# Kernel optimization log

Hardware: AMD Instinct MI355X
Metric: run time of the kernel (lower is better)

## Reference

```python
import jax, jax.numpy as jnp
import numpy as np

N_NODES = 50000
N_EDGES = 800000
D = 128


def setup_inputs() -> dict:
    key = jax.random.key(0)
    ks = jax.random.split(key, 8)
    scale = 1.0 / np.sqrt(D)
    return {
        "x": jax.random.normal(ks[0], (N_NODES, D), jnp.float32),
        "src": jax.random.randint(ks[1], (N_EDGES,), 0, N_NODES, jnp.int64 if jax.config.jax_enable_x64 else jnp.int32),
        "dst": jax.random.randint(ks[2], (N_EDGES,), 0, N_NODES, jnp.int64 if jax.config.jax_enable_x64 else jnp.int32),
        "W_self0": jax.random.normal(ks[3], (D, D), jnp.float32) * scale,
        "W_neigh0": jax.random.normal(ks[4], (D, D), jnp.float32) * scale,
        "b0": jnp.zeros((D,), jnp.float32),
        "W_self1": jax.random.normal(ks[5], (D, D), jnp.float32) * scale,
        "W_neigh1": jax.random.normal(ks[6], (D, D), jnp.float32) * scale,
        "b1": jnp.zeros((D,), jnp.float32),
    }


def _sage_conv(h, src, dst, W_self, W_neigh, b, n_nodes):
    # mean aggregation over incoming edges (DGL copy_u + mean; isolated nodes -> 0)
    msg = h[src]                                             # [E, d]
    agg = jax.ops.segment_sum(msg, dst, num_segments=n_nodes)  # [N, d]
    deg = jax.ops.segment_sum(jnp.ones((src.shape[0],), h.dtype), dst, num_segments=n_nodes)
    h_neigh = agg / jnp.maximum(deg, 1.0)[:, None]
    return h @ W_self + h_neigh @ W_neigh + b


def reference(x, src, dst, W_self0, W_neigh0, b0, W_self1, W_neigh1, b1):
    n = x.shape[0]
    h = jax.nn.relu(_sage_conv(x, src, dst, W_self0, W_neigh0, b0, n))
    h = jax.nn.relu(_sage_conv(h, src, dst, W_self1, W_neigh1, b1, n))
    # torch F.normalize(p=2, dim=1): x / max(||x||_2, eps)
    norm = jnp.sqrt(jnp.sum(h * h, axis=1, keepdims=True))
    return h / jnp.maximum(norm, 1e-12)
```

## Files before the change

### kernel.cpp

```cpp
#include <hip/hip_runtime.h>

#define NN 50000
#define D 128
#define BM 32
#define SL 6250
#define CE 1664

typedef unsigned int uint;
typedef unsigned short ushort;
typedef __attribute__((ext_vector_type(8))) short bf16x8;
typedef __attribute__((ext_vector_type(4))) float f32x4;

static __device__ __forceinline__ ushort f2bf(float f) {
    uint u = __float_as_uint(f);
    u = (u + 0x7FFFu + ((u >> 16) & 1u)) >> 16;
    return (ushort)u;
}

#define ADD8(a, u)                                                  \
    {                                                               \
        a[0] += __uint_as_float((u).x << 16);                       \
        a[1] += __uint_as_float((u).x & 0xFFFF0000u);               \
        a[2] += __uint_as_float((u).y << 16);                       \
        a[3] += __uint_as_float((u).y & 0xFFFF0000u);               \
        a[4] += __uint_as_float((u).z << 16);                       \
        a[5] += __uint_as_float((u).z & 0xFFFF0000u);               \
        a[6] += __uint_as_float((u).w << 16);                       \
        a[7] += __uint_as_float((u).w & 0xFFFF0000u);               \
    }

static __device__ __forceinline__ int ladr(int r, int ch) {
    return r * D + (((ch) ^ (r & 7)) << 3);
}

__global__ __launch_bounds__(256) void k_hist_s(const int* __restrict__ dst,
                                                int* __restrict__ hist, int E) {
    const int s = blockIdx.x & 7;
    const int lo = s * SL, hi = lo + SL;
    const int bs = blockIdx.x >> 3;
    for (int e = bs * 256 + (int)threadIdx.x; e < E; e += 128 * 256) {
        const int d = dst[e];
        if (d >= lo && d < hi) atomicAdd(&hist[d], 1);
    }
}

__global__ __launch_bounds__(256) void k_bsum(const int* __restrict__ hist,
                                              int* __restrict__ bsum, int n) {
    const int t = threadIdx.x;
    const int i0 = blockIdx.x * 512 + t * 2;
    int s = 0;
    if (i0 < n) s += hist[i0];
    if (i0 + 1 < n) s += hist[i0 + 1];
    #pragma unroll
    for (int o = 1; o < 64; o <<= 1) s += __shfl_xor(s, o);
    __shared__ int wsum[4];
    if ((t & 63) == 0) wsum[t >> 6] = s;
    __syncthreads();
    if (t == 0) bsum[blockIdx.x] = wsum[0] + wsum[1] + wsum[2] + wsum[3];
}

__global__ __launch_bounds__(256) void k_scanapply_f(
    const int* __restrict__ hist, const int* __restrict__ bsum,
    int* __restrict__ row_off, int* __restrict__ cursor, int n, int E, int nb,
    const float* __restrict__ x, ushort* __restrict__ xb,
    const float* __restrict__ W0, const float* __restrict__ W1,
    const float* __restrict__ W2, const float* __restrict__ W3,
    ushort* __restrict__ P)
{
    const int bid = blockIdx.x;
    const int t = threadIdx.x;
    if (bid < nb) {
        const int sb = bid;
        const int lane = t & 63, w = t >> 6;
        __shared__ int red[4], wsum[4], woff[4], baseS;

        int v = (t < nb && t < sb) ? bsum[t] : 0;
        #pragma unroll
        for (int o = 1; o < 64; o <<= 1) v += __shfl_xor(v, o);
        if (lane == 0) red[w] = v;
        __syncthreads();
        if (t == 0) baseS = red[0] + red[1] + red[2] + red[3];
        __syncthreads();
        const int base = baseS;

        const int i0 = sb * 512 + t * 2;
        const int v0 = (i0 < n) ? hist[i0] : 0;
        const int v1 = (i0 + 1 < n) ? hist[i0 + 1] : 0;
        const int s = v0 + v1;
        int inc = s;
        #pragma unroll
        for (int o = 1; o < 64; o <<= 1) { int u = __shfl_up(inc, o); if (lane >= o) inc += u; }
        if (lane == 63) wsum[w] = inc;
        __syncthreads();
        if (t == 0) { int r = 0; for (int k = 0; k < 4; ++k) { woff[k] = r; r += wsum[k]; } }
        __syncthreads();
        const int ex = base + woff[w] + (inc - s);
        if (i0 < n)     { row_off[i0] = ex;          cursor[i0] = ex; }
        if (i0 + 1 < n) { row_off[i0 + 1] = ex + v0; cursor[i0 + 1] = ex + v0; }
        if (sb == 0 && t == 0) row_off[n] = E;
    } else if (bid < nb + 3125) {
        const int tt = (bid - nb) * 256 + t;
        const float4* p = reinterpret_cast<const float4*>(x) + (size_t)tt * 2;
        const float4 v0 = p[0], v1 = p[1];
        uint4 u;
        u.x = (uint)f2bf(v0.x) | ((uint)f2bf(v0.y) << 16);
        u.y = (uint)f2bf(v0.z) | ((uint)f2bf(v0.w) << 16);
        u.z = (uint)f2bf(v1.x) | ((uint)f2bf(v1.y) << 16);
        u.w = (uint)f2bf(v1.z) | ((uint)f2bf(v1.w) << 16);
        reinterpret_cast<uint4*>(xb)[tt] = u;
    } else {
        const int o = (bid - nb - 3125) * 256 + t;
        const int mat = o >> 14;
        const int idx = o & 16383;
        const int kt = idx >> 12;
        const int nn = (idx >> 5) & 127;
        const int ks = idx & 31;
        const float* W = (mat == 0) ? W0 : (mat == 1) ? W1 : (mat == 2) ? W2 : W3;
        P[o] = f2bf(W[(kt * 32 + ks) * D + nn]);
    }
}

__global__ __launch_bounds__(256) void k_fill_s(const int* __restrict__ src,
        const int* __restrict__ dst, int* __restrict__ cursor,
        int* __restrict__ csr, int E) {
    const int s = blockIdx.x & 7;
    const int lo = s * SL, hi = lo + SL;
    const int bs = blockIdx.x >> 3;
    const int stride = (gridDim.x >> 3) * 256;
    for (int e = bs * 256 + (int)threadIdx.x; e < E; e += stride) {
        const int d = dst[e];
        const int sv = src[e];
        if (d >= lo && d < hi) {
            const int p = atomicAdd(&cursor[d], 1);
            csr[p] = sv;
        }
    }
}

template<bool NORM>
__global__ __launch_bounds__(512, 8) void k_sage(
    const ushort* __restrict__ hb,
    const int* __restrict__ csr, const int* __restrict__ row_off,
    const ushort* __restrict__ Wps, const ushort* __restrict__ Wpn,
    const float* __restrict__ bias, ushort* __restrict__ outb,
    float* __restrict__ out, int n, int E)
{
    __shared__ __align__(16) ushort hsb[BM * D];
    __shared__ __align__(16) ushort hnb[BM * D];
    __shared__ float outt[BM * 132];
    __shared__ int csre[CE];
    const int row0 = blockIdx.x * BM;
    const int tid = threadIdx.x;
    const int l = tid & 63;
    const int w = tid >> 6;

    const int rhi = min(row0 + BM, n);
    const int beg0 = row_off[row0];
    const int EB = row_off[rhi] - beg0;
    const bool useLds = (EB <= CE);
    if (useLds) {
        for (int j = tid; j < EB; j += 512) csre[j] = csr[beg0 + j];
    }

    {
        const int r = tid >> 4;
        const int ch = tid & 15;
        const int g = row0 + r;
        uint4 u = make_uint4(0u, 0u, 0u, 0u);
        if (g < n) u = *reinterpret_cast<const uint4*>(hb + (size_t)g * D + ch * 8);
        *reinterpret_cast<uint4*>(&hsb[ladr(r, ch)]) = u;
    }
    __syncthreads();

    {
        const int r = tid >> 4;
        const int ql = tid & 15;
        const int g = row0 + r;
        int i = 0, e = 0;
        if (g < n) { i = row_off[g]; e = row_off[g + 1]; }
        const float invd = (e > i) ? 1.0f / (float)(e - i) : 0.0f;
        float a[8];
        #pragma unroll
        for (int j = 0; j < 8; ++j) a[j] = 0.f;
        const size_t off = (size_t)(ql * 8);
        if (useLds) {
            int li = i - beg0;
            const int le = e - beg0;
            for (; li + 3 < le; li += 4) {
                const int s0 = csre[li], s1 = csre[li + 1], s2 = csre[li + 2], s3 = csre[li + 3];
                const uint4 u0 = *reinterpret_cast<const uint4*>(hb + (size_t)s0 * D + off);
                const uint4 u1 = *reinterpret_cast<const uint4*>(hb + (size_t)s1 * D + off);
                const uint4 u2 = *reinterpret_cast<const uint4*>(hb + (size_t)s2 * D + off);
                const uint4 u3 = *reinterpret_cast<const uint4*>(hb + (size_t)s3 * D + off);
                ADD8(a, u0); ADD8(a, u1); ADD8(a, u2); ADD8(a, u3);
            }
            for (; li < le; ++li) {
                const int s0 = csre[li];
                const uint4 u0 = *reinterpret_cast<const uint4*>(hb + (size_t)s0 * D + off);
                ADD8(a, u0);
            }
        } else {
            for (; i + 3 < e; i += 4) {
                const int s0 = csr[i], s1 = csr[i + 1], s2 = csr[i + 2], s3 = csr[i + 3];
                const uint4 u0 = *reinterpret_cast<const uint4*>(hb + (size_t)s0 * D + off);
                const uint4 u1 = *reinterpret_cast<const uint4*>(hb + (size_t)s1 * D + off);
                const uint4 u2 = *reinterpret_cast<const uint4*>(hb + (size_t)s2 * D + off);
                const uint4 u3 = *reinterpret_cast<const uint4*>(hb + (size_t)s3 * D + off);
                ADD8(a, u0); ADD8(a, u1); ADD8(a, u2); ADD8(a, u3);
            }
            for (; i < e; ++i) {
                const int s0 = csr[i];
                const uint4 u0 = *reinterpret_cast<const uint4*>(hb + (size_t)s0 * D + off);
                ADD8(a, u0);
            }
        }
        uint4 u;
        u.x = (uint)f2bf(a[0] * invd) | ((uint)f2bf(a[1] * invd) << 16);
        u.y = (uint)f2bf(a[2] * invd) | ((uint)f2bf(a[3] * invd) << 16);
        u.z = (uint)f2bf(a[4] * invd) | ((uint)f2bf(a[5] * invd) << 16);
        u.w = (uint)f2bf(a[6] * invd) | ((uint)f2bf(a[7] * invd) << 16);
        *reinterpret_cast<uint4*>(&hnb[ladr(r, ql)]) = u;
    }
    __syncthreads();

    {
        const int mt = w >> 2;
        const int ntA = (w & 3) * 2;
        const int rA = mt * 16 + (l & 15);
        const int kg = l >> 4;
        f32x4 acc0 = {0.f, 0.f, 0.f, 0.f};
        f32x4 acc1 = {0.f, 0.f, 0.f, 0.f};
        #pragma unroll
        for (int kt = 0; kt < 4; ++kt) {
            const int kc = kt * 4 + kg;
            const bf16x8 as = *reinterpret_cast<const bf16x8*>(&hsb[ladr(rA, kc)]);
            const bf16x8 an = *reinterpret_cast<const bf16x8*>(&hnb[ladr(rA, kc)]);
            const size_t wo0 = (size_t)(kt * 128 + ntA * 16 + (l & 15)) * 32 + kg * 8;
            const size_t wo1 = wo0 + 16 * 32;
            const bf16x8 bs0 = *reinterpret_cast<const bf16x8*>(Wps + wo0);
            const bf16x8 bn0 = *reinterpret_cast<const bf16x8*>(Wpn + wo0);
            const bf16x8 bs1 = *reinterpret_cast<const bf16x8*>(Wps + wo1);
            const bf16x8 bn1 = *reinterpret_cast<const bf16x8*>(Wpn + wo1);
            acc0 = __builtin_amdgcn_mfma_f32_16x16x32_bf16(as, bs0, acc0, 0, 0, 0);
            acc0 = __builtin_amdgcn_mfma_f32_16x16x32_bf16(an, bn0, acc0, 0, 0, 0);
            acc1 = __builtin_amdgcn_mfma_f32_16x16x32_bf16(as, bs1, acc1, 0, 0, 0);
            acc1 = __builtin_amdgcn_mfma_f32_16x16x32_bf16(an, bn1, acc1, 0, 0, 0);
        }
        const int c0 = ntA * 16 + (l & 15);
        const float bv0 = bias[c0], bv1 = bias[c0 + 16];
        #pragma unroll
        for (int i2 = 0; i2 < 4; ++i2) {
            const int rr = mt * 16 + kg * 4 + i2;
            outt[rr * 132 + c0]      = fmaxf(acc0[i2] + bv0, 0.f);
            outt[rr * 132 + c0 + 16] = fmaxf(acc1[i2] + bv1, 0.f);
        }
    }
    __syncthreads();

    {
        const int r = tid >> 4;
        const int c = (tid & 15) * 8;
        const int g = row0 + r;
        float4 v0 = *reinterpret_cast<const float4*>(&outt[r * 132 + c]);
        float4 v1 = *reinterpret_cast<const float4*>(&outt[r * 132 + c + 4]);
        if (!NORM) {
            if (g < n) {
                uint4 u;
                u.x = (uint)f2bf(v0.x) | ((uint)f2bf(v0.y) << 16);
                u.y = (uint)f2bf(v0.z) | ((uint)f2bf(v0.w) << 16);
                u.z = (uint)f2bf(v1.x) | ((uint)f2bf(v1.y) << 16);
                u.w = (uint)f2bf(v1.z) | ((uint)f2bf(v1.w) << 16);
                *reinterpret_cast<uint4*>(outb + (size_t)g * D + c) = u;
            }
        } else {
            float ssq = v0.x * v0.x + v0.y * v0.y + v0.z * v0.z + v0.w * v0.w
                      + v1.x * v1.x + v1.y * v1.y + v1.z * v1.z + v1.w * v1.w;
            #pragma unroll
            for (int o = 1; o < 16; o <<= 1) ssq += __shfl_xor(ssq, o);
            const float scale = 1.0f / fmaxf(sqrtf(ssq), 1e-12f);
            if (g < n) {
                v0.x *= scale; v0.y *= scale; v0.z *= scale; v0.w *= scale;
                v1.x *= scale; v1.y *= scale; v1.z *= scale; v1.w *= scale;
                *reinterpret_cast<float4*>(out + (size_t)g * D + c)     = v0;
                *reinterpret_cast<float4*>(out + (size_t)g * D + c + 4) = v1;
            }
        }
    }
}

extern "C" void kernel_launch(void* const* d_in, const int* in_sizes, int n_in,
                              void* d_out, int out_size, void* d_ws, size_t ws_size,
                              hipStream_t stream) {
    const float* x   = (const float*)d_in[0];
    const int*   src = (const int*)d_in[1];
    const int*   dst = (const int*)d_in[2];
    const float* Ws0 = (const float*)d_in[3];
    const float* Wn0 = (const float*)d_in[4];
    const float* b0  = (const float*)d_in[5];
    const float* Ws1 = (const float*)d_in[6];
    const float* Wn1 = (const float*)d_in[7];
    const float* b1  = (const float*)d_in[8];
    float* out = (float*)d_out;
    const int E = in_sizes[1];

    ushort* xb     = (ushort*)d_ws;
    ushort* h1b    = xb + (size_t)NN * D;
    ushort* Wp     = h1b + (size_t)NN * D;
    int*    hist   = (int*)(Wp + 65536);
    int*    bsum   = hist + NN;
    int*    row_off= bsum + 128;
    int*    cursor = row_off + NN + 1;
    int*    csr    = cursor + NN;

    ushort* Wps0 = Wp;
    ushort* Wpn0 = Wp + 16384;
    ushort* Wps1 = Wp + 32768;
    ushort* Wpn1 = Wp + 49152;

    const int nb = (NN + 511) / 512;

    hipMemsetAsync(hist, 0, (size_t)NN * sizeof(int), stream);
    k_hist_s<<<1024, 256, 0, stream>>>(dst, hist, E);
    k_bsum<<<nb, 256, 0, stream>>>(hist, bsum, NN);
    k_scanapply_f<<<nb + 3125 + 256, 256, 0, stream>>>(
        hist, bsum, row_off, cursor, NN, E, nb,
        x, xb, Ws0, Wn0, Ws1, Wn1, Wp);
    k_fill_s<<<1024, 256, 0, stream>>>(src, dst, cursor, csr, E);

    k_sage<false><<<(NN + BM - 1) / BM, 512, 0, stream>>>(
        xb, csr, row_off, Wps0, Wpn0, b0, h1b, nullptr, NN, E);

    k_sage<true><<<(NN + BM - 1) / BM, 512, 0, stream>>>(
        h1b, csr, row_off, Wps1, Wpn1, b1, nullptr, out, NN, E);
}
```

Measured before the change: 171.8 us.

## Privatize degree histogram into eight copies and unroll LDS gather by eight

The histogram kernel previously had each block re-read all of dst and filter to one of eight node slices. It now reads each edge once and does an atomic add into one of eight private histogram copies chosen by block index. The bsum kernel reduces the eight copies into the final histogram. The aim is to avoid reading dst eight times and to spread atomic contention, at the cost of an eight-times-larger memset and an extra reduction read. Separately, the LDS-index neighbor gather loop gets an 8-way unrolled stage so more loads are in flight.

```diff
diff --git a/kernel.cpp b/kernel.cpp
--- a/kernel.cpp
+++ b/kernel.cpp
@@ -33,24 +33,29 @@
     return r * D + (((ch) ^ (r & 7)) << 3);
 }
 
-__global__ __launch_bounds__(256) void k_hist_s(const int* __restrict__ dst,
-                                                int* __restrict__ hist, int E) {
-    const int s = blockIdx.x & 7;
-    const int lo = s * SL, hi = lo + SL;
-    const int bs = blockIdx.x >> 3;
-    for (int e = bs * 256 + (int)threadIdx.x; e < E; e += 128 * 256) {
-        const int d = dst[e];
-        if (d >= lo && d < hi) atomicAdd(&hist[d], 1);
-    }
-}
-
-__global__ __launch_bounds__(256) void k_bsum(const int* __restrict__ hist,
-                                              int* __restrict__ bsum, int n) {
+__global__ __launch_bounds__(256) void k_hist8(const int* __restrict__ dst,
+                                               int* __restrict__ hist8, int E) {
+    int* h = hist8 + (blockIdx.x & 7) * NN;
+    for (int e = blockIdx.x * 256 + (int)threadIdx.x; e < E; e += 1024 * 256)
+        atomicAdd(&h[dst[e]], 1);
+}
+
+__global__ __launch_bounds__(256) void k_bsum(const int* __restrict__ hist8,
+        int* __restrict__ hist, int* __restrict__ bsum, int n) {
     const int t = threadIdx.x;
     const int i0 = blockIdx.x * 512 + t * 2;
     int s = 0;
-    if (i0 < n) s += hist[i0];
-    if (i0 + 1 < n) s += hist[i0 + 1];
+    #pragma unroll
+    for (int k = 0; k < 2; ++k) {
+        const int i = i0 + k;
+        if (i < n) {
+            int v = 0;
+            #pragma unroll
+            for (int c = 0; c < 8; ++c) v += hist8[c * NN + i];
+            hist[i] = v;
+            s += v;
+        }
+    }
     #pragma unroll
     for (int o = 1; o < 64; o <<= 1) s += __shfl_xor(s, o);
     __shared__ int wsum[4];
@@ -186,6 +191,20 @@
         if (useLds) {
             int li = i - beg0;
             const int le = e - beg0;
+            for (; li + 7 < le; li += 8) {
+                const int s0 = csre[li],     s1 = csre[li + 1], s2 = csre[li + 2], s3 = csre[li + 3];
+                const int s4 = csre[li + 4], s5 = csre[li + 5], s6 = csre[li + 6], s7 = csre[li + 7];
+                const uint4 u0 = *reinterpret_cast<const uint4*>(hb + (size_t)s0 * D + off);
+                const uint4 u1 = *reinterpret_cast<const uint4*>(hb + (size_t)s1 * D + off);
+                const uint4 u2 = *reinterpret_cast<const uint4*>(hb + (size_t)s2 * D + off);
+                const uint4 u3 = *reinterpret_cast<const uint4*>(hb + (size_t)s3 * D + off);
+                const uint4 u4 = *reinterpret_cast<const uint4*>(hb + (size_t)s4 * D + off);
+                const uint4 u5 = *reinterpret_cast<const uint4*>(hb + (size_t)s5 * D + off);
+                const uint4 u6 = *reinterpret_cast<const uint4*>(hb + (size_t)s6 * D + off);
+                const uint4 u7 = *reinterpret_cast<const uint4*>(hb + (size_t)s7 * D + off);
+                ADD8(a, u0); ADD8(a, u1); ADD8(a, u2); ADD8(a, u3);
+                ADD8(a, u4); ADD8(a, u5); ADD8(a, u6); ADD8(a, u7);
+            }
             for (; li + 3 < le; li += 4) {
                 const int s0 = csre[li], s1 = csre[li + 1], s2 = csre[li + 2], s3 = csre[li + 3];
                 const uint4 u0 = *reinterpret_cast<const uint4*>(hb + (size_t)s0 * D + off);
@@ -306,7 +325,8 @@
     ushort* xb     = (ushort*)d_ws;
     ushort* h1b    = xb + (size_t)NN * D;
     ushort* Wp     = h1b + (size_t)NN * D;
-    int*    hist   = (int*)(Wp + 65536);
+    int*    hist8  = (int*)(Wp + 65536);
+    int*    hist   = hist8 + 8 * NN;
     int*    bsum   = hist + NN;
     int*    row_off= bsum + 128;
     int*    cursor = row_off + NN + 1;
@@ -319,9 +339,9 @@
 
     const int nb = (NN + 511) / 512;
 
-    hipMemsetAsync(hist, 0, (size_t)NN * sizeof(int), stream);
-    k_hist_s<<<1024, 256, 0, stream>>>(dst, hist, E);
-    k_bsum<<<nb, 256, 0, stream>>>(hist, bsum, NN);
+    hipMemsetAsync(hist8, 0, (size_t)8 * NN * sizeof(int), stream);
+    k_hist8<<<1024, 256, 0, stream>>>(dst, hist8, E);
+    k_bsum<<<nb, 256, 0, stream>>>(hist8, hist, bsum, NN);
     k_scanapply_f<<<nb + 3125 + 256, 256, 0, stream>>>(
         hist, bsum, row_off, cursor, NN, E, nb,
         x, xb, Ws0, Wn0, Ws1, Wn1, Wp);
```

After: 213.9 us. 24.5% more time.
